# Optimization experiments

Measured on AMD Instinct MI355X. Metric: run time of the kernel, lower is better.

## Reference

```python
import jax, jax.numpy as jnp
import numpy as np
from jax import lax

PATCH = 3  # also hist_window since n_history = 1


def setup_inputs() -> dict:
    key = jax.random.key(0)
    k1, k2, k3 = jax.random.split(key, 3)
    B, Seq, F = 128, 3000, 64
    x = jax.random.normal(k1, (B, Seq, F), dtype=jnp.float32)
    agg_w = jax.random.normal(k2, (PATCH, PATCH), dtype=jnp.float32)  # Linear(hist_window=3 -> patch=3)
    agg_b = jax.random.normal(k3, (PATCH,), dtype=jnp.float32)
    return {"x": x, "agg_w": agg_w, "agg_b": agg_b}


def reference(x, agg_w, agg_b):
    # DDI forward with alpha=0.0 (default): for each patch i,
    #   prev   = output[:, i-patch:i, :]            (previous produced patch)
    #   agg    = gelu(Linear(prev.permute(0,2,1))).permute(0,2,1)
    #   output[:, i:i+patch, :] = agg + x[:, i:i+patch, :]
    # Dropout is identity (eval). Strict sequential dep -> lax.scan over chunks.
    B, Seq, F = x.shape
    head = x[:, :PATCH, :]  # first hist_window tokens copied through
    n_chunks = (Seq - PATCH) // PATCH  # 999
    # [n_chunks, B, patch, F]
    chunks = jnp.swapaxes(x[:, PATCH:, :].reshape(B, n_chunks, PATCH, F), 0, 1)

    def step(prev, cur):
        # prev, cur: [B, patch, F]
        # Linear over history axis: out[b,p,f] = sum_h prev[b,h,f] * W[p,h] + b[p]
        agg = jnp.einsum('bhf,ph->bpf', prev, agg_w) + agg_b[None, :, None]
        agg = jax.nn.gelu(agg, approximate=False)  # torch F.gelu default is exact
        res = agg + cur
        return res, res

    _, out_chunks = lax.scan(step, head, chunks)  # [n_chunks, B, patch, F]
    tail = jnp.swapaxes(out_chunks, 0, 1).reshape(B, Seq - PATCH, F)
    return jnp.concatenate([head, tail], axis=1)
```

## Files before the change

kernel.cpp:

```cpp
#include <hip/hip_runtime.h>
#include <math.h>

#define SEQ   3000
#define FDIM  64

#define PPW  0.23164189f
#define B1c  0.127414796f
#define B2c  (-0.142248368f)
#define B3c  0.7107068705f
#define B4c  (-0.7265760135f)
#define B5c  0.5307027145f
#define NL2E (-0.72134752044448170368f)

#define DPPF(src, ctrl)                                                       \
    __builtin_bit_cast(float, __builtin_amdgcn_update_dpp(                    \
        0, __builtin_bit_cast(int, (src)), (ctrl), 0xf, 0xf, false))

#define DECL9(p) float p##0,p##1,p##2,p##3,p##4,p##5,p##6,p##7,p##8
#define TOUCH9(P) "+v"(P##0),"+v"(P##1),"+v"(P##2),"+v"(P##3),"+v"(P##4),     \
    "+v"(P##5),"+v"(P##6),"+v"(P##7),"+v"(P##8)

#define PF1(dst, p, OFF)                                                      \
    asm volatile("global_load_dword %0, %1, off offset:" #OFF                 \
                 : "=v"(dst) : "v"(p) : "memory")
#define ST1(val, p, OFF)                                                      \
    asm volatile("global_store_dword %0, %1, off offset:" #OFF                \
                 :: "v"(p), "v"(val) : "memory")

#define PF9(P) do {                                                           \
    PF1(P##0, xc, 0); PF1(P##1, xc, 768); PF1(P##2, xc, 1536);                \
    xc += 9 * FDIM;                                                           \
    PF1(P##3, xc, 0); PF1(P##4, xc, 768); PF1(P##5, xc, 1536);                \
    xc += 9 * FDIM;                                                           \
    PF1(P##6, xc, 0); PF1(P##7, xc, 768); PF1(P##8, xc, 1536);                \
    xc += 9 * FDIM;                                                           \
} while (0)

#define WAITVM(Nlit, P) do {                                                  \
    asm volatile("s_waitcnt vmcnt(" #Nlit ")" : TOUCH9(P) : : "memory");      \
    __builtin_amdgcn_sched_barrier(0);                                        \
} while (0)

#define GSTEP(F, u) do {                                                      \
    int si_ = __builtin_bit_cast(int, s);                                     \
    float d1_ = __builtin_bit_cast(float,                                     \
        __builtin_amdgcn_update_dpp(0, si_, 9,  0xf, 0xf, false));            \
    float d2_ = __builtin_bit_cast(float,                                     \
        __builtin_amdgcn_update_dpp(0, si_, 82, 0xf, 0xf, false));            \
    float a_ = fmaf(wA, s, q);                                                \
    a_ = fmaf(wB, d1_, a_);                                                   \
    a_ = fmaf(wC, d2_, a_);                                                   \
    float m_ = (a_ * a_) * NL2E;                                              \
    float e_ = __builtin_amdgcn_exp2f(m_);                                    \
    float ab_ = fabsf(a_);                                                    \
    float dd_ = fmaf(PPW, ab_, 1.0f);                                         \
    float r_ = __builtin_amdgcn_rcpf(dd_);                                    \
    float p_ = fmaf(B2c, r_, B1c);                                            \
    float n_ = fmaf(B4c, r_, B3c);                                            \
    float rr_ = r_ * r_;                                                      \
    p_ = fmaf(n_, rr_, p_);                                                   \
    float r4_ = rr_ * rr_;                                                    \
    p_ = fmaf(B5c, r4_, p_);                                                  \
    float er_ = (p_ * r_) * e_;                                               \
    s = fmaf(-ab_, er_, fmaxf(a_, 0.0f)) + u;                                 \
    ST1(s, oc, F);                                                            \
} while (0)

#define COMPUTE_GRP(P) do {                                                   \
    GSTEP(0, P##0); GSTEP(768, P##1); GSTEP(1536, P##2);  oc += 9 * FDIM;     \
    GSTEP(0, P##3); GSTEP(768, P##4); GSTEP(1536, P##5);  oc += 9 * FDIM;     \
    GSTEP(0, P##6); GSTEP(768, P##7); GSTEP(1536, P##8);  oc += 9 * FDIM;     \
} while (0)

__global__ __launch_bounds__(64, 1) void scan_kernel(
    const float* __restrict__ x,
    const float* __restrict__ w,
    const float* __restrict__ bias,
    float* __restrict__ out)
{
    const int lane = threadIdx.x;
    const int g  = lane >> 2;
    const int pr = lane & 3;
    const int p  = pr < 3 ? pr : 2;

    const int b = blockIdx.x >> 2;
    const int f = ((blockIdx.x & 3) << 4) + g;

    const int p1 = (p + 1) == 3 ? 0 : p + 1;
    const int p2 = (p + 2) >= 3 ? p - 1 : p + 2;
    float wA = w[p * 3 + p];
    float wB = w[p * 3 + p1];
    float wC = w[p * 3 + p2];
    float q  = bias[p];

    const float* __restrict__ xp = x   + (size_t)b * (SEQ * FDIM) + (size_t)p * FDIM + f;
    float*       __restrict__ op = out + (size_t)b * (SEQ * FDIM) + (size_t)p * FDIM + f;

    float s = xp[0];
    asm volatile("" : "+v"(s), "+v"(wA), "+v"(wB), "+v"(wC), "+v"(q));
    ST1(s, op, 0);

    const float* xc = xp + 3 * FDIM;
    float*       oc = op + 3 * FDIM;

    DECL9(LA); DECL9(LB);

    PF9(LA);
    PF9(LB);
    WAITVM(9, LA);

    #pragma unroll 1
    for (int t = 0; t < 54; ++t) {
        COMPUTE_GRP(LA);
        PF9(LA);
        WAITVM(18, LB);
        COMPUTE_GRP(LB);
        PF9(LB);
        WAITVM(18, LA);
    }

    COMPUTE_GRP(LA);
    PF9(LA);
    WAITVM(18, LB);
    COMPUTE_GRP(LB);
    WAITVM(9, LA);
    COMPUTE_GRP(LA);
}

extern "C" void kernel_launch(void* const* d_in, const int* in_sizes, int n_in,
                              void* d_out, int out_size, void* d_ws, size_t ws_size,
                              hipStream_t stream) {
    const float* x    = (const float*)d_in[0];
    const float* w    = (const float*)d_in[1];
    const float* bias = (const float*)d_in[2];
    float* out        = (float*)d_out;

    hipLaunchKernelGGL(scan_kernel, dim3(512), dim3(64), 0, stream,
                       x, w, bias, out);
}
```

Baseline: 61.86 us.

## Split linear term to shorten serial dependency chain and remap blocks to XCDs

The recurrence is rewritten so the linear mix of the previous state is split. The part from the input u (the W·u plus bias term) is computed one step ahead off the critical path, and only W·gelu_prev is added on the chain. This removes the add-then-DPP latency from each serial step. The GELU tail is also reordered so more terms are computed in parallel with the reciprocal, and block indices are remapped so neighbouring batches and features spread across XCDs differently. It adds extra DPP and FMA work per step, and the numerics change slightly because of the reassociation.

```diff
diff --git a/kernel.cpp b/kernel.cpp
--- a/kernel.cpp
+++ b/kernel.cpp
@@ -12,9 +12,8 @@
 #define B5c  0.5307027145f
 #define NL2E (-0.72134752044448170368f)
 
-#define DPPF(src, ctrl)                                                       \
-    __builtin_bit_cast(float, __builtin_amdgcn_update_dpp(                    \
-        0, __builtin_bit_cast(int, (src)), (ctrl), 0xf, 0xf, false))
+#define DPPI(srci, ctrl)                                                      \
+    __builtin_amdgcn_update_dpp(0, (srci), (ctrl), 0xf, 0xf, false)
 
 #define DECL9(p) float p##0,p##1,p##2,p##3,p##4,p##5,p##6,p##7,p##8
 #define TOUCH9(P) "+v"(P##0),"+v"(P##1),"+v"(P##2),"+v"(P##3),"+v"(P##4),     \
@@ -42,28 +41,36 @@
 } while (0)
 
 #define GSTEP(F, u) do {                                                      \
-    int si_ = __builtin_bit_cast(int, s);                                     \
-    float d1_ = __builtin_bit_cast(float,                                     \
-        __builtin_amdgcn_update_dpp(0, si_, 9,  0xf, 0xf, false));            \
-    float d2_ = __builtin_bit_cast(float,                                     \
-        __builtin_amdgcn_update_dpp(0, si_, 82, 0xf, 0xf, false));            \
-    float a_ = fmaf(wA, s, q);                                                \
+               \
+    int ui_ = __builtin_bit_cast(int, u);                                     \
+    float ud1_ = __builtin_bit_cast(float, DPPI(ui_, 9));                     \
+    float ud2_ = __builtin_bit_cast(float, DPPI(ui_, 82));                    \
+    float qn_ = fmaf(wA, u, q);                                               \
+    qn_ = fmaf(wB, ud1_, qn_);                                                \
+    qn_ = fmaf(wC, ud2_, qn_);                                                \
+                                                          \
+    int gi_ = __builtin_bit_cast(int, gc);                                    \
+    float d1_ = __builtin_bit_cast(float, DPPI(gi_, 9));                      \
+    float d2_ = __builtin_bit_cast(float, DPPI(gi_, 82));                     \
+    float a_ = fmaf(wA, gc, qe);                                              \
     a_ = fmaf(wB, d1_, a_);                                                   \
     a_ = fmaf(wC, d2_, a_);                                                   \
     float m_ = (a_ * a_) * NL2E;                                              \
     float e_ = __builtin_amdgcn_exp2f(m_);                                    \
-    float ab_ = fabsf(a_);                                                    \
-    float dd_ = fmaf(PPW, ab_, 1.0f);                                         \
+    float z_ = (-fabsf(a_)) * e_;                          \
+    float dd_ = fmaf(PPW, fabsf(a_), 1.0f);                                   \
     float r_ = __builtin_amdgcn_rcpf(dd_);                                    \
-    float p_ = fmaf(B2c, r_, B1c);                                            \
-    float n_ = fmaf(B4c, r_, B3c);                                            \
+    float c01_ = fmaf(B2c, r_, B1c);                                          \
+    float c23_ = fmaf(B4c, r_, B3c);                                          \
     float rr_ = r_ * r_;                                                      \
-    p_ = fmaf(n_, rr_, p_);                                                   \
     float r4_ = rr_ * rr_;                                                    \
+    float p_ = fmaf(c23_, rr_, c01_);                                         \
     p_ = fmaf(B5c, r4_, p_);                                                  \
-    float er_ = (p_ * r_) * e_;                                               \
-    s = fmaf(-ab_, er_, fmaxf(a_, 0.0f)) + u;                                 \
-    ST1(s, oc, F);                                                            \
+    float pr_ = p_ * r_;                                                      \
+    gc = fmaf(pr_, z_, fmaxf(a_, 0.0f));                             \
+    float s_ = gc + u;                                    \
+    ST1(s_, oc, F);                                                           \
+    qe = qn_;                                                                 \
 } while (0)
 
 #define COMPUTE_GRP(P) do {                                                   \
@@ -83,8 +90,12 @@
     const int pr = lane & 3;
     const int p  = pr < 3 ? pr : 2;
 
-    const int b = blockIdx.x >> 2;
-    const int f = ((blockIdx.x & 3) << 4) + g;
+    const int B = blockIdx.x;
+    const int xs = B & 7, h = (B >> 3) & 1, j = B >> 4;
+    const int i = j * 8 + xs;
+    const int b = i >> 1;
+    const int fq = ((i & 1) << 1) | h;
+    const int f = (fq << 4) + g;
 
     const int p1 = (p + 1) == 3 ? 0 : p + 1;
     const int p2 = (p + 2) >= 3 ? p - 1 : p + 2;
@@ -96,9 +107,10 @@
     const float* __restrict__ xp = x   + (size_t)b * (SEQ * FDIM) + (size_t)p * FDIM + f;
     float*       __restrict__ op = out + (size_t)b * (SEQ * FDIM) + (size_t)p * FDIM + f;
 
-    float s = xp[0];
-    asm volatile("" : "+v"(s), "+v"(wA), "+v"(wB), "+v"(wC), "+v"(q));
-    ST1(s, op, 0);
+    float gc = xp[0];
+    asm volatile("" : "+v"(gc), "+v"(wA), "+v"(wB), "+v"(wC), "+v"(q));
+    ST1(gc, op, 0);
+    float qe = q;
 
     const float* xc = xp + 3 * FDIM;
     float*       oc = op + 3 * FDIM;
```

After: 72.32 us. +16.9%, slower.
